# Optimization experiments

Hardware: AMD Instinct MI355X
Metric: run time of the kernel (lower is better)

The kernel has to match this reference:

```python
import jax, jax.numpy as jnp
import numpy as np

LEAKY_SLOPE = 0.01

def bilinear_interpolate(grid, coords):
    # grid: [H, W, C]; coords: [N, 2] in [0,1] (x, y order as in torch code)
    H = grid.shape[0] - 1
    W = grid.shape[1] - 1
    fx = coords[:, 0] * W
    fy = coords[:, 1] * H
    x0 = fx.astype(jnp.int32)
    y0 = fy.astype(jnp.int32)
    xf = jnp.mod(fx, 1.0)
    yf = jnp.mod(fy, 1.0)
    x1 = jnp.minimum(x0 + 1, W)
    y1 = jnp.minimum(y0 + 1, H)
    tl = grid[y0, x0]  # [N, C]
    tr = grid[y0, x1]
    bl = grid[y1, x0]
    br = grid[y1, x1]
    xf = xf[:, None]
    yf = yf[:, None]
    top = (1.0 - xf) * tl + xf * tr
    bot = (1.0 - xf) * bl + xf * br
    return (1.0 - yf) * top + yf * bot


def setup_inputs() -> dict:
    key = jax.random.key(0)
    ks = jax.random.split(key, 10)
    N = 2097152
    pos = jax.random.uniform(ks[0], (N, 2), dtype=jnp.float32)
    dir = jax.random.uniform(ks[1], (N, 2), dtype=jnp.float32)
    pos_grid = jax.random.normal(ks[2], (256, 256, 3), dtype=jnp.float32) * 10.0
    dir_grid = jax.random.normal(ks[3], (256, 256, 3), dtype=jnp.float32) * 10.0
    # Linear layers: PyTorch default init U(-1/sqrt(fan_in), 1/sqrt(fan_in))
    def linear(kw, kb, fan_in, fan_out):
        bound = 1.0 / np.sqrt(fan_in)
        W = jax.random.uniform(kw, (fan_out, fan_in), minval=-bound, maxval=bound, dtype=jnp.float32)
        b = jax.random.uniform(kb, (fan_out,), minval=-bound, maxval=bound, dtype=jnp.float32)
        return W, b
    W1, b1 = linear(ks[4], ks[5], 6, 64)
    W2, b2 = linear(ks[6], ks[7], 64, 64)
    W3, b3 = linear(ks[8], ks[9], 64, 1)
    return {"pos": pos, "dir": dir, "pos_grid": pos_grid, "dir_grid": dir_grid,
            "W1": W1, "b1": b1, "W2": W2, "b2": b2, "W3": W3, "b3": b3}


def reference(pos, dir, pos_grid, dir_grid, W1, b1, W2, b2, W3, b3):
    pos_feat = jax.lax.stop_gradient(bilinear_interpolate(pos_grid, pos))  # .detach() in torch
    dir_feat = jax.lax.stop_gradient(bilinear_interpolate(dir_grid, dir))
    x = jnp.concatenate([pos_feat, dir_feat], axis=1)  # [N, 6]
    x = jax.nn.leaky_relu(x @ W1.T + b1, LEAKY_SLOPE)
    x = jax.nn.leaky_relu(x @ W2.T + b2, LEAKY_SLOPE)
    return jax.nn.sigmoid(x @ W3.T + b3)  # [N, 1]
```

## Files before the change

### kernel.cpp

```cpp
#include <hip/hip_runtime.h>
#include <hip/hip_bf16.h>
#include <math.h>


#define NTHREADS 256

typedef __attribute__((ext_vector_type(4))) short s16x4;
typedef __attribute__((ext_vector_type(8))) short s16x8;
typedef __attribute__((ext_vector_type(8))) __bf16 bf16x8;
typedef __attribute__((ext_vector_type(4))) float f32x4;
typedef __attribute__((ext_vector_type(4))) int i32x4;
typedef __attribute__((ext_vector_type(2))) int i32x2;

static __device__ __forceinline__ short f2bf(float f) {
    return __builtin_bit_cast(short, __float2bfloat16(f));
}
static __device__ __forceinline__ int pk2(float lo, float hi) {
    unsigned short l = (unsigned short)f2bf(lo);
    unsigned short h = (unsigned short)f2bf(hi);
    return (int)(((unsigned int)h << 16) | (unsigned int)l);
}
static __device__ __forceinline__ int cvt_pk_bf16(float a, float b) {
    int r;
    asm("v_cvt_pk_bf16_f32 %0, %1, %2" : "=v"(r) : "v"(a), "v"(b));
    return r;
}
static __device__ __forceinline__ float bflo(int u) {
    return __builtin_bit_cast(float, u << 16);
}
static __device__ __forceinline__ float bfhi(int u) {
    return __builtin_bit_cast(float, (int)(u & 0xffff0000));
}
static __device__ __forceinline__ int opaq(int x) {
    asm volatile("" : "+v"(x));
    return x;
}

__global__ __launch_bounds__(256) void make_patches(
    const float* __restrict__ gP, const float* __restrict__ gD,
    int* __restrict__ outP, int* __restrict__ outD) {
    int gid = blockIdx.x * 256 + threadIdx.x;
    const float* g = (gid < 65536) ? gP : gD;
    int* po = (gid < 65536) ? outP : outD;
    int id = gid & 65535;
    int y0 = id >> 8, x0 = id & 255;
    int x1 = min(x0 + 1, 255), y1 = min(y0 + 1, 255);
    const float* tl = g + (y0 * 256 + x0) * 3;
    const float* tr = g + (y0 * 256 + x1) * 3;
    const float* bl = g + (y1 * 256 + x0) * 3;
    const float* br = g + (y1 * 256 + x1) * 3;
    i32x4 u0;
    i32x2 u1;
    u0[0] = pk2(tl[0], bl[0]);
    u0[1] = pk2(tl[1], bl[1]);
    u0[2] = pk2(tl[2], bl[2]);
    u0[3] = pk2(tr[0], br[0]);
    u1[0] = pk2(tr[1], br[1]);
    u1[1] = pk2(tr[2], br[2]);
    *(i32x4*)(po + id * 8) = u0;
    *(i32x2*)(po + id * 8 + 4) = u1;
}

__global__ void pack_weights(const float* __restrict__ W1,
                             const float* __restrict__ b1,
                             const float* __restrict__ W2,
                             int* __restrict__ wt1, int* __restrict__ wt2) {
    int lane = threadIdx.x;
    int c = lane & 15, q = lane >> 4, q4 = q * 4;
#pragma unroll
    for (int mt = 0; mt < 4; ++mt) {
        int f = mt * 16 + c;
        float v[4];
#pragma unroll
        for (int j = 0; j < 4; ++j) {
            int k = q4 + j;
            float x = 0.0f;
            if (k < 6) x = W1[f * 6 + k];
            else if (k == 6) x = b1[f];
            v[j] = x;
        }
        wt1[lane * 8 + mt * 2 + 0] = pk2(v[0], v[1]);
        wt1[lane * 8 + mt * 2 + 1] = pk2(v[2], v[3]);
    }
#pragma unroll
    for (int kt2 = 0; kt2 < 2; ++kt2)
#pragma unroll
        for (int mt = 0; mt < 4; ++mt) {
            int n2 = mt * 16 + c;
            float v[8];
#pragma unroll
            for (int j2 = 0; j2 < 8; ++j2) {
                int k = kt2 * 32 + ((j2 >> 2) * 16) + q4 + (j2 & 3);
                v[j2] = W2[n2 * 64 + k];
            }
            int base = lane * 32 + (kt2 * 4 + mt) * 4;
#pragma unroll
            for (int h = 0; h < 4; ++h)
                wt2[base + h] = pk2(v[2 * h], v[2 * h + 1]);
        }
}

static __device__ __forceinline__ void patch_issue(
    const int* __restrict__ tab, float px, float py, int* P, float& xf,
    float& yf) {
    float fx = px * 255.0f;
    float fy = py * 255.0f;
    int x0 = (int)fx;
    int y0 = (int)fy;
    xf = fx - floorf(fx);
    yf = fy - floorf(fy);
    int idx = (y0 << 8) | x0;
    i32x4 a = *(const i32x4*)(tab + idx * 8);
    i32x2 b = *(const i32x2*)(tab + idx * 8 + 4);
    P[0] = a[0]; P[1] = a[1]; P[2] = a[2];
    P[3] = a[3]; P[4] = b[0]; P[5] = b[1];
}

static __device__ __forceinline__ void patch_lerp(const int* P, float xf,
                                                  float yf, float* f) {
#pragma unroll
    for (int ch = 0; ch < 3; ++ch) {
        float tl = bflo(P[ch]), bl = bfhi(P[ch]);
        float tr = bflo(P[ch + 3]), br = bfhi(P[ch + 3]);
        float top = fmaf(xf, tr - tl, tl);
        float bot = fmaf(xf, br - bl, bl);
        f[ch] = fmaf(yf, bot - top, top);
    }
}

__global__ __launch_bounds__(NTHREADS, 5) void mlp_mfma_kernel(
    const float* __restrict__ pos, const float* __restrict__ dir,
    const int* __restrict__ patP, const int* __restrict__ patD,
    const int* __restrict__ wt1, const int* __restrict__ wt2,
    const float* __restrict__ b2, const float* __restrict__ W3,
    const float* __restrict__ b3, float* __restrict__ out) {
    __shared__ int lds_F[4 * 64 * 4];
    __shared__ __align__(16) float cw[128];

    const int tid = threadIdx.x;
    if (tid < 128) cw[tid] = (tid < 64) ? b2[tid] : W3[tid - 64];
    __syncthreads();

    const int w = tid >> 6;
    const int lane = tid & 63;
    const int c = lane & 15;
    const int q = lane >> 4;
    const int q4 = q * 4;

    int* FB = lds_F + w * (64 * 4);

    s16x4 A1f[4];
#pragma unroll
    for (int mt = 0; mt < 4; ++mt)
        A1f[mt] = __builtin_bit_cast(
            s16x4, *(const i32x2*)(wt1 + lane * 8 + mt * 2));
    s16x8 A2f[2][4];
#pragma unroll
    for (int kt2 = 0; kt2 < 2; ++kt2)
#pragma unroll
        for (int mt = 0; mt < 4; ++mt)
            A2f[kt2][mt] = __builtin_bit_cast(
                s16x8,
                *(const i32x4*)(wt2 + lane * 32 + (kt2 * 4 + mt) * 4));

    const float b3s = b3[0];
    const int dbias = pk2(1.0f, 0.0f);
    const f32x4 zacc = {0.f, 0.f, 0.f, 0.f};

    const long base = ((long)blockIdx.x * 4 + w) * 64;
    const float2* pos2 = (const float2*)pos;
    const float2* dir2 = (const float2*)dir;

    {
        float2 cp = pos2[base + lane];
        float2 cd = dir2[base + lane];
        int P0_[12];
        float fr0[4];
        patch_issue(patP, cp.x, cp.y, P0_, fr0[0], fr0[1]);
        patch_issue(patD, cd.x, cd.y, P0_ + 6, fr0[2], fr0[3]);
        float feat[6];
        patch_lerp(P0_, fr0[0], fr0[1], feat);
        patch_lerp(P0_ + 6, fr0[2], fr0[3], feat + 3);
        i32x4 dv;
        dv[0] = cvt_pk_bf16(feat[0], feat[1]);
        dv[1] = cvt_pk_bf16(feat[2], feat[3]);
        dv[2] = cvt_pk_bf16(feat[4], feat[5]);
        dv[3] = dbias;
        *(i32x4*)(FB + lane * 4) = dv;
    }

    float s[4];
#pragma unroll
    for (int t = 0; t < 4; ++t) {
        i32x2 bi = *(const i32x2*)(FB + (t * 16 + c) * 4 + (q & 1) * 2);
        s16x4 bfeat = __builtin_bit_cast(s16x4, bi);

        f32x4 a1[4];
#pragma unroll
        for (int mt = 0; mt < 4; ++mt)
            a1[mt] = __builtin_amdgcn_mfma_f32_16x16x16bf16_1k(
                A1f[mt], bfeat, zacc, 0, 0, 0);

        i32x4 bbi[2];
#pragma unroll
        for (int kt2 = 0; kt2 < 2; ++kt2)
#pragma unroll
            for (int h = 0; h < 2; ++h) {
                f32x4 x = a1[kt2 * 2 + h];
                float l0 = fmaxf(x[0], 0.01f * x[0]);
                float l1 = fmaxf(x[1], 0.01f * x[1]);
                float l2 = fmaxf(x[2], 0.01f * x[2]);
                float l3 = fmaxf(x[3], 0.01f * x[3]);
                bbi[kt2][h * 2 + 0] = cvt_pk_bf16(l0, l1);
                bbi[kt2][h * 2 + 1] = cvt_pk_bf16(l2, l3);
            }

        f32x4 a2[4];
        {
            const float* cwb = cw + opaq(q4);
#pragma unroll
            for (int mt = 0; mt < 4; ++mt)
                a2[mt] = *(const f32x4*)(cwb + mt * 16);
        }
#pragma unroll
        for (int kt2 = 0; kt2 < 2; ++kt2) {
            bf16x8 bb = __builtin_bit_cast(bf16x8, bbi[kt2]);
#pragma unroll
            for (int mt = 0; mt < 4; ++mt)
                a2[mt] = __builtin_amdgcn_mfma_f32_16x16x32_bf16(
                    __builtin_bit_cast(bf16x8, A2f[kt2][mt]), bb, a2[mt],
                    0, 0, 0);
        }

        float tx = 0.0f, ta = 0.0f;
        const float* cww = cw + opaq(64 + q4);
#pragma unroll
        for (int mt = 0; mt < 4; ++mt) {
            const f32x4 wv = *(const f32x4*)(cww + mt * 16);
#pragma unroll
            for (int r = 0; r < 4; ++r) {
                float x = a2[mt][r];
                tx = fmaf(x, wv[r], tx);
                ta = fmaf(__builtin_fabsf(x), wv[r], ta);
            }
        }
        float tt = fmaf(0.505f, tx, 0.495f * ta);
        tt += __shfl_xor(tt, 16, 64);
        tt += __shfl_xor(tt, 32, 64);
        s[t] = tt;
    }

    float sa = (q & 1) ? s[1] : s[0];
    float sb = (q & 1) ? s[3] : s[2];
    float v = (q & 2) ? sb : sa;
    v += b3s;
    v = 1.0f / (1.0f + __expf(-v));
    out[base + q * 16 + c] = v;
}

extern "C" void kernel_launch(void* const* d_in, const int* in_sizes, int n_in,
                              void* d_out, int out_size, void* d_ws,
                              size_t ws_size, hipStream_t stream) {
    const float* pos = (const float*)d_in[0];
    const float* dir = (const float*)d_in[1];
    const float* pos_grid = (const float*)d_in[2];
    const float* dir_grid = (const float*)d_in[3];
    const float* W1 = (const float*)d_in[4];
    const float* b1 = (const float*)d_in[5];
    const float* W2 = (const float*)d_in[6];
    const float* b2 = (const float*)d_in[7];
    const float* W3 = (const float*)d_in[8];
    const float* b3 = (const float*)d_in[9];
    float* out = (float*)d_out;

    int* patP = (int*)d_ws;
    int* patD = patP + 65536 * 8;
    int* wt1 = patD + 65536 * 8;
    int* wt2 = wt1 + 512;

    make_patches<<<512, 256, 0, stream>>>(pos_grid, dir_grid, patP, patD);
    pack_weights<<<1, 64, 0, stream>>>(W1, b1, W2, wt1, wt2);

    const int n = in_sizes[0] / 2;
    const int batches = n / 64;
    const int blocks = batches / 4;

    mlp_mfma_kernel<<<blocks, NTHREADS, 0, stream>>>(
        pos, dir, patP, patD, wt1, wt2, b2, W3, b3, out);
}
```

Baseline: 154.5 us.

## Process four 64-point batches per wave with prefetched coordinates and packed math

Each wave now loops over four 64-point batches, which spreads the per-wave weight and bias setup over more work and cuts the grid to a quarter of its size. The next batch's pos/dir loads are issued before the current batch's lerp and MFMA work so their latency is hidden. The layer-2 bias moves from LDS into registers, and the leaky-relu and final dot product use packed v_pk_mul/v_pk_fma plus v_fract instead of floor. The extra registers lower the launch-bounds occupancy hint from 5 to 4, and with fewer blocks there is less parallelism left to hide gather latency.

```diff
diff --git a/kernel.cpp b/kernel.cpp
--- a/kernel.cpp
+++ b/kernel.cpp
@@ -4,11 +4,13 @@
 
 
 #define NTHREADS 256
+#define NB 4
 
 typedef __attribute__((ext_vector_type(4))) short s16x4;
 typedef __attribute__((ext_vector_type(8))) short s16x8;
 typedef __attribute__((ext_vector_type(8))) __bf16 bf16x8;
 typedef __attribute__((ext_vector_type(4))) float f32x4;
+typedef __attribute__((ext_vector_type(2))) float f32x2;
 typedef __attribute__((ext_vector_type(4))) int i32x4;
 typedef __attribute__((ext_vector_type(2))) int i32x2;
 
@@ -23,6 +25,21 @@
 static __device__ __forceinline__ int cvt_pk_bf16(float a, float b) {
     int r;
     asm("v_cvt_pk_bf16_f32 %0, %1, %2" : "=v"(r) : "v"(a), "v"(b));
+    return r;
+}
+static __device__ __forceinline__ f32x2 pk_fma(f32x2 a, f32x2 b, f32x2 c) {
+    f32x2 d;
+    asm("v_pk_fma_f32 %0, %1, %2, %3" : "=v"(d) : "v"(a), "v"(b), "v"(c));
+    return d;
+}
+static __device__ __forceinline__ f32x2 pk_mul(f32x2 a, f32x2 b) {
+    f32x2 d;
+    asm("v_pk_mul_f32 %0, %1, %2" : "=v"(d) : "v"(a), "v"(b));
+    return d;
+}
+static __device__ __forceinline__ float fractf_hw(float x) {
+    float r;
+    asm("v_fract_f32 %0, %1" : "=v"(r) : "v"(x));
     return r;
 }
 static __device__ __forceinline__ float bflo(int u) {
@@ -107,8 +124,8 @@
     float fy = py * 255.0f;
     int x0 = (int)fx;
     int y0 = (int)fy;
-    xf = fx - floorf(fx);
-    yf = fy - floorf(fy);
+    xf = fractf_hw(fx);
+    yf = fractf_hw(fy);
     int idx = (y0 << 8) | x0;
     i32x4 a = *(const i32x4*)(tab + idx * 8);
     i32x2 b = *(const i32x2*)(tab + idx * 8 + 4);
@@ -128,17 +145,17 @@
     }
 }
 
-__global__ __launch_bounds__(NTHREADS, 5) void mlp_mfma_kernel(
+__global__ __launch_bounds__(NTHREADS, 4) void mlp_mfma_kernel(
     const float* __restrict__ pos, const float* __restrict__ dir,
     const int* __restrict__ patP, const int* __restrict__ patD,
     const int* __restrict__ wt1, const int* __restrict__ wt2,
     const float* __restrict__ b2, const float* __restrict__ W3,
     const float* __restrict__ b3, float* __restrict__ out) {
     __shared__ int lds_F[4 * 64 * 4];
-    __shared__ __align__(16) float cw[128];
+    __shared__ __align__(16) float cw[64];
 
     const int tid = threadIdx.x;
-    if (tid < 128) cw[tid] = (tid < 64) ? b2[tid] : W3[tid - 64];
+    if (tid < 64) cw[tid] = W3[tid];
     __syncthreads();
 
     const int w = tid >> 6;
@@ -162,100 +179,125 @@
             A2f[kt2][mt] = __builtin_bit_cast(
                 s16x8,
                 *(const i32x4*)(wt2 + lane * 32 + (kt2 * 4 + mt) * 4));
+    f32x4 ci[4];
+#pragma unroll
+    for (int mt = 0; mt < 4; ++mt)
+        ci[mt] = *(const f32x4*)(b2 + mt * 16 + q4);
 
     const float b3s = b3[0];
     const int dbias = pk2(1.0f, 0.0f);
-    const f32x4 zacc = {0.f, 0.f, 0.f, 0.f};
-
-    const long base = ((long)blockIdx.x * 4 + w) * 64;
+    const f32x2 c001 = {0.01f, 0.01f};
+
+    const long wave_global = (long)blockIdx.x * 4 + w;
+    const long base0 = wave_global * (64L * NB);
     const float2* pos2 = (const float2*)pos;
     const float2* dir2 = (const float2*)dir;
 
-    {
-        float2 cp = pos2[base + lane];
-        float2 cd = dir2[base + lane];
+    float2 cp = pos2[base0 + lane];
+    float2 cd = dir2[base0 + lane];
+
+#pragma unroll 1
+    for (int ib = 0; ib < NB; ++ib) {
+        const long base = base0 + ib * 64;
+
         int P0_[12];
         float fr0[4];
         patch_issue(patP, cp.x, cp.y, P0_, fr0[0], fr0[1]);
         patch_issue(patD, cd.x, cd.y, P0_ + 6, fr0[2], fr0[3]);
-        float feat[6];
-        patch_lerp(P0_, fr0[0], fr0[1], feat);
-        patch_lerp(P0_ + 6, fr0[2], fr0[3], feat + 3);
-        i32x4 dv;
-        dv[0] = cvt_pk_bf16(feat[0], feat[1]);
-        dv[1] = cvt_pk_bf16(feat[2], feat[3]);
-        dv[2] = cvt_pk_bf16(feat[4], feat[5]);
-        dv[3] = dbias;
-        *(i32x4*)(FB + lane * 4) = dv;
+
+        {
+            int mb = min(ib + 1, NB - 1);
+            cp = pos2[base0 + mb * 64 + lane];
+            cd = dir2[base0 + mb * 64 + lane];
+        }
+
+        {
+            float feat[6];
+            patch_lerp(P0_, fr0[0], fr0[1], feat);
+            patch_lerp(P0_ + 6, fr0[2], fr0[3], feat + 3);
+            i32x4 dv;
+            dv[0] = cvt_pk_bf16(feat[0], feat[1]);
+            dv[1] = cvt_pk_bf16(feat[2], feat[3]);
+            dv[2] = cvt_pk_bf16(feat[4], feat[5]);
+            dv[3] = dbias;
+            *(i32x4*)(FB + lane * 4) = dv;
+        }
+
+        float s[4];
+#pragma unroll
+        for (int t = 0; t < 4; ++t) {
+            i32x2 bi = *(const i32x2*)(FB + (t * 16 + c) * 4 + (q & 1) * 2);
+            s16x4 bfeat = __builtin_bit_cast(s16x4, bi);
+
+            const f32x4 zacc = {0.f, 0.f, 0.f, 0.f};
+            f32x4 a1[4];
+#pragma unroll
+            for (int mt = 0; mt < 4; ++mt)
+                a1[mt] = __builtin_amdgcn_mfma_f32_16x16x16bf16_1k(
+                    A1f[mt], bfeat, zacc, 0, 0, 0);
+
+            i32x4 bbi[2];
+#pragma unroll
+            for (int kt2 = 0; kt2 < 2; ++kt2)
+#pragma unroll
+                for (int h = 0; h < 2; ++h) {
+                    f32x4 x = a1[kt2 * 2 + h];
+                    f32x2 xlo = {x[0], x[1]}, xhi = {x[2], x[3]};
+                    f32x2 ylo = pk_mul(xlo, c001);
+                    f32x2 yhi = pk_mul(xhi, c001);
+                    float l0 = fmaxf(x[0], ylo[0]);
+                    float l1 = fmaxf(x[1], ylo[1]);
+                    float l2 = fmaxf(x[2], yhi[0]);
+                    float l3 = fmaxf(x[3], yhi[1]);
+                    bbi[kt2][h * 2 + 0] = cvt_pk_bf16(l0, l1);
+                    bbi[kt2][h * 2 + 1] = cvt_pk_bf16(l2, l3);
+                }
+
+            f32x4 a2[4];
+#pragma unroll
+            for (int mt = 0; mt < 4; ++mt) a2[mt] = ci[mt];
+#pragma unroll
+            for (int kt2 = 0; kt2 < 2; ++kt2) {
+                bf16x8 bb = __builtin_bit_cast(bf16x8, bbi[kt2]);
+#pragma unroll
+                for (int mt = 0; mt < 4; ++mt)
+                    a2[mt] = __builtin_amdgcn_mfma_f32_16x16x32_bf16(
+                        __builtin_bit_cast(bf16x8, A2f[kt2][mt]), bb, a2[mt],
+                        0, 0, 0);
+            }
+
+            f32x2 tx = {0.f, 0.f}, ta = {0.f, 0.f};
+            const float* cww = cw + opaq(q4);
+#pragma unroll
+            for (int mt = 0; mt < 4; ++mt) {
+                const f32x4 wv = *(const f32x4*)(cww + mt * 16);
+                f32x2 w0 = {wv[0], wv[1]}, w1 = {wv[2], wv[3]};
+                f32x4 x = a2[mt];
+                i32x4 xb = __builtin_bit_cast(i32x4, x);
+                i32x4 ab = {xb[0] & 0x7fffffff, xb[1] & 0x7fffffff,
+                            xb[2] & 0x7fffffff, xb[3] & 0x7fffffff};
+                f32x4 xa = __builtin_bit_cast(f32x4, ab);
+                f32x2 xlo = {x[0], x[1]}, xhi = {x[2], x[3]};
+                f32x2 alo = {xa[0], xa[1]}, ahi = {xa[2], xa[3]};
+                tx = pk_fma(xlo, w0, tx);
+                tx = pk_fma(xhi, w1, tx);
+                ta = pk_fma(alo, w0, ta);
+                ta = pk_fma(ahi, w1, ta);
+            }
+            float tt = fmaf(0.505f, tx[0] + tx[1],
+                            0.495f * (ta[0] + ta[1]));
+            tt += __shfl_xor(tt, 16, 64);
+            tt += __shfl_xor(tt, 32, 64);
+            s[t] = tt;
+        }
+
+        float sa = (q & 1) ? s[1] : s[0];
+        float sb = (q & 1) ? s[3] : s[2];
+        float v = (q & 2) ? sb : sa;
+        v += b3s;
+        v = 1.0f / (1.0f + __expf(-v));
+        out[base + q * 16 + c] = v;
     }
-
-    float s[4];
-#pragma unroll
-    for (int t = 0; t < 4; ++t) {
-        i32x2 bi = *(const i32x2*)(FB + (t * 16 + c) * 4 + (q & 1) * 2);
-        s16x4 bfeat = __builtin_bit_cast(s16x4, bi);
-
-        f32x4 a1[4];
-#pragma unroll
-        for (int mt = 0; mt < 4; ++mt)
-            a1[mt] = __builtin_amdgcn_mfma_f32_16x16x16bf16_1k(
-                A1f[mt], bfeat, zacc, 0, 0, 0);
-
-        i32x4 bbi[2];
-#pragma unroll
-        for (int kt2 = 0; kt2 < 2; ++kt2)
-#pragma unroll
-            for (int h = 0; h < 2; ++h) {
-                f32x4 x = a1[kt2 * 2 + h];
-                float l0 = fmaxf(x[0], 0.01f * x[0]);
-                float l1 = fmaxf(x[1], 0.01f * x[1]);
-                float l2 = fmaxf(x[2], 0.01f * x[2]);
-                float l3 = fmaxf(x[3], 0.01f * x[3]);
-                bbi[kt2][h * 2 + 0] = cvt_pk_bf16(l0, l1);
-                bbi[kt2][h * 2 + 1] = cvt_pk_bf16(l2, l3);
-            }
-
-        f32x4 a2[4];
-        {
-            const float* cwb = cw + opaq(q4);
-#pragma unroll
-            for (int mt = 0; mt < 4; ++mt)
-                a2[mt] = *(const f32x4*)(cwb + mt * 16);
-        }
-#pragma unroll
-        for (int kt2 = 0; kt2 < 2; ++kt2) {
-            bf16x8 bb = __builtin_bit_cast(bf16x8, bbi[kt2]);
-#pragma unroll
-            for (int mt = 0; mt < 4; ++mt)
-                a2[mt] = __builtin_amdgcn_mfma_f32_16x16x32_bf16(
-                    __builtin_bit_cast(bf16x8, A2f[kt2][mt]), bb, a2[mt],
-                    0, 0, 0);
-        }
-
-        float tx = 0.0f, ta = 0.0f;
-        const float* cww = cw + opaq(64 + q4);
-#pragma unroll
-        for (int mt = 0; mt < 4; ++mt) {
-            const f32x4 wv = *(const f32x4*)(cww + mt * 16);
-#pragma unroll
-            for (int r = 0; r < 4; ++r) {
-                float x = a2[mt][r];
-                tx = fmaf(x, wv[r], tx);
-                ta = fmaf(__builtin_fabsf(x), wv[r], ta);
-            }
-        }
-        float tt = fmaf(0.505f, tx, 0.495f * ta);
-        tt += __shfl_xor(tt, 16, 64);
-        tt += __shfl_xor(tt, 32, 64);
-        s[t] = tt;
-    }
-
-    float sa = (q & 1) ? s[1] : s[0];
-    float sb = (q & 1) ? s[3] : s[2];
-    float v = (q & 2) ? sb : sa;
-    v += b3s;
-    v = 1.0f / (1.0f + __expf(-v));
-    out[base + q * 16 + c] = v;
 }
 
 extern "C" void kernel_launch(void* const* d_in, const int* in_sizes, int n_in,
@@ -283,7 +325,8 @@
 
     const int n = in_sizes[0] / 2;
     const int batches = n / 64;
-    const int blocks = batches / 4;
+    const int waves = batches / NB;
+    const int blocks = waves / 4;
 
     mlp_mfma_kernel<<<blocks, NTHREADS, 0, stream>>>(
         pos, dir, patP, patD, wt1, wt2, b2, W3, b3, out);
```

Measured after the change: 142.4 us. 7.9% less time.

## Software-pipeline patch gathers across batches per wave and fuse setup kernels

Applied to the files above, without the earlier changes.

Each wave now processes four 64-point batches in a loop. It issues the grid-patch gathers and the coordinate loads for upcoming batches before running the MFMA MLP on the current one, so gather latency overlaps compute. The weight-packing kernel is merged into the patch-building kernel to save a launch. b2 is held in registers instead of LDS, and frac uses v_fract_f32. The kernel launches a quarter as many blocks with occupancy bound lowered to 4, which raises register pressure and reduces parallelism.

```diff
diff --git a/kernel.cpp b/kernel.cpp
--- a/kernel.cpp
+++ b/kernel.cpp
@@ -4,6 +4,7 @@
 
 
 #define NTHREADS 256
+#define NB 4
 
 typedef __attribute__((ext_vector_type(4))) short s16x4;
 typedef __attribute__((ext_vector_type(8))) short s16x8;
@@ -25,6 +26,11 @@
     asm("v_cvt_pk_bf16_f32 %0, %1, %2" : "=v"(r) : "v"(a), "v"(b));
     return r;
 }
+static __device__ __forceinline__ float fractf_hw(float x) {
+    float r;
+    asm("v_fract_f32 %0, %1" : "=v"(r) : "v"(x));
+    return r;
+}
 static __device__ __forceinline__ float bflo(int u) {
     return __builtin_bit_cast(float, u << 16);
 }
@@ -38,66 +44,65 @@
 
 __global__ __launch_bounds__(256) void make_patches(
     const float* __restrict__ gP, const float* __restrict__ gD,
-    int* __restrict__ outP, int* __restrict__ outD) {
+    const float* __restrict__ W1, const float* __restrict__ b1,
+    const float* __restrict__ W2, int* __restrict__ outP,
+    int* __restrict__ outD, int* __restrict__ wt1, int* __restrict__ wt2) {
     int gid = blockIdx.x * 256 + threadIdx.x;
-    const float* g = (gid < 65536) ? gP : gD;
-    int* po = (gid < 65536) ? outP : outD;
-    int id = gid & 65535;
-    int y0 = id >> 8, x0 = id & 255;
-    int x1 = min(x0 + 1, 255), y1 = min(y0 + 1, 255);
-    const float* tl = g + (y0 * 256 + x0) * 3;
-    const float* tr = g + (y0 * 256 + x1) * 3;
-    const float* bl = g + (y1 * 256 + x0) * 3;
-    const float* br = g + (y1 * 256 + x1) * 3;
-    i32x4 u0;
-    i32x2 u1;
-    u0[0] = pk2(tl[0], bl[0]);
-    u0[1] = pk2(tl[1], bl[1]);
-    u0[2] = pk2(tl[2], bl[2]);
-    u0[3] = pk2(tr[0], br[0]);
-    u1[0] = pk2(tr[1], br[1]);
-    u1[1] = pk2(tr[2], br[2]);
-    *(i32x4*)(po + id * 8) = u0;
-    *(i32x2*)(po + id * 8 + 4) = u1;
-}
-
-__global__ void pack_weights(const float* __restrict__ W1,
-                             const float* __restrict__ b1,
-                             const float* __restrict__ W2,
-                             int* __restrict__ wt1, int* __restrict__ wt2) {
-    int lane = threadIdx.x;
-    int c = lane & 15, q = lane >> 4, q4 = q * 4;
-#pragma unroll
-    for (int mt = 0; mt < 4; ++mt) {
-        int f = mt * 16 + c;
-        float v[4];
-#pragma unroll
-        for (int j = 0; j < 4; ++j) {
-            int k = q4 + j;
-            float x = 0.0f;
-            if (k < 6) x = W1[f * 6 + k];
-            else if (k == 6) x = b1[f];
-            v[j] = x;
+    if (gid < 131072) {
+        const float* g = (gid < 65536) ? gP : gD;
+        int* po = (gid < 65536) ? outP : outD;
+        int id = gid & 65535;
+        int y0 = id >> 8, x0 = id & 255;
+        int x1 = min(x0 + 1, 255), y1 = min(y0 + 1, 255);
+        const float* tl = g + (y0 * 256 + x0) * 3;
+        const float* tr = g + (y0 * 256 + x1) * 3;
+        const float* bl = g + (y1 * 256 + x0) * 3;
+        const float* br = g + (y1 * 256 + x1) * 3;
+        i32x4 u0;
+        i32x2 u1;
+        u0[0] = pk2(tl[0], bl[0]);
+        u0[1] = pk2(tl[1], bl[1]);
+        u0[2] = pk2(tl[2], bl[2]);
+        u0[3] = pk2(tr[0], br[0]);
+        u1[0] = pk2(tr[1], br[1]);
+        u1[1] = pk2(tr[2], br[2]);
+        *(i32x4*)(po + id * 8) = u0;
+        *(i32x2*)(po + id * 8 + 4) = u1;
+    } else if (gid < 131136) {
+        int lane = gid - 131072;
+        int c = lane & 15, q = lane >> 4, q4 = q * 4;
+#pragma unroll
+        for (int mt = 0; mt < 4; ++mt) {
+            int f = mt * 16 + c;
+            float v[4];
+#pragma unroll
+            for (int j = 0; j < 4; ++j) {
+                int k = q4 + j;
+                float x = 0.0f;
+                if (k < 6) x = W1[f * 6 + k];
+                else if (k == 6) x = b1[f];
+                v[j] = x;
+            }
+            wt1[lane * 8 + mt * 2 + 0] = pk2(v[0], v[1]);
+            wt1[lane * 8 + mt * 2 + 1] = pk2(v[2], v[3]);
         }
-        wt1[lane * 8 + mt * 2 + 0] = pk2(v[0], v[1]);
-        wt1[lane * 8 + mt * 2 + 1] = pk2(v[2], v[3]);
+#pragma unroll
+        for (int kt2 = 0; kt2 < 2; ++kt2)
+#pragma unroll
+            for (int mt = 0; mt < 4; ++mt) {
+                int n2 = mt * 16 + c;
+                float v[8];
+#pragma unroll
+                for (int j2 = 0; j2 < 8; ++j2) {
+                    int k = kt2 * 32 + ((j2 >> 2) * 16) + q4 + (j2 & 3);
+                    v[j2] = W2[n2 * 64 + k];
+                }
+                int base = lane * 32 + (kt2 * 4 + mt) * 4;
+#pragma unroll
+                for (int h = 0; h < 4; ++h)
+                    wt2[base + h] = pk2(v[2 * h], v[2 * h + 1]);
+            }
     }
-#pragma unroll
-    for (int kt2 = 0; kt2 < 2; ++kt2)
-#pragma unroll
-        for (int mt = 0; mt < 4; ++mt) {
-            int n2 = mt * 16 + c;
-            float v[8];
-#pragma unroll
-            for (int j2 = 0; j2 < 8; ++j2) {
-                int k = kt2 * 32 + ((j2 >> 2) * 16) + q4 + (j2 & 3);
-                v[j2] = W2[n2 * 64 + k];
-            }
-            int base = lane * 32 + (kt2 * 4 + mt) * 4;
-#pragma unroll
-            for (int h = 0; h < 4; ++h)
-                wt2[base + h] = pk2(v[2 * h], v[2 * h + 1]);
-        }
 }
 
 static __device__ __forceinline__ void patch_issue(
@@ -107,8 +112,8 @@
     float fy = py * 255.0f;
     int x0 = (int)fx;
     int y0 = (int)fy;
-    xf = fx - floorf(fx);
-    yf = fy - floorf(fy);
+    xf = fractf_hw(fx);
+    yf = fractf_hw(fy);
     int idx = (y0 << 8) | x0;
     i32x4 a = *(const i32x4*)(tab + idx * 8);
     i32x2 b = *(const i32x2*)(tab + idx * 8 + 4);
@@ -128,17 +133,17 @@
     }
 }
 
-__global__ __launch_bounds__(NTHREADS, 5) void mlp_mfma_kernel(
+__global__ __launch_bounds__(NTHREADS, 4) void mlp_mfma_kernel(
     const float* __restrict__ pos, const float* __restrict__ dir,
     const int* __restrict__ patP, const int* __restrict__ patD,
     const int* __restrict__ wt1, const int* __restrict__ wt2,
     const float* __restrict__ b2, const float* __restrict__ W3,
     const float* __restrict__ b3, float* __restrict__ out) {
     __shared__ int lds_F[4 * 64 * 4];
-    __shared__ __align__(16) float cw[128];
+    __shared__ __align__(16) float cw[64];
 
     const int tid = threadIdx.x;
-    if (tid < 128) cw[tid] = (tid < 64) ? b2[tid] : W3[tid - 64];
+    if (tid < 64) cw[tid] = W3[tid];
     __syncthreads();
 
     const int w = tid >> 6;
@@ -162,22 +167,28 @@
             A2f[kt2][mt] = __builtin_bit_cast(
                 s16x8,
                 *(const i32x4*)(wt2 + lane * 32 + (kt2 * 4 + mt) * 4));
+    f32x4 ci[4];
+#pragma unroll
+    for (int mt = 0; mt < 4; ++mt)
+        ci[mt] = *(const f32x4*)(b2 + mt * 16 + q4);
 
     const float b3s = b3[0];
     const int dbias = pk2(1.0f, 0.0f);
-    const f32x4 zacc = {0.f, 0.f, 0.f, 0.f};
-
-    const long base = ((long)blockIdx.x * 4 + w) * 64;
+
+    const long wave_global = (long)blockIdx.x * 4 + w;
+    const long base0 = wave_global * (64L * NB);
     const float2* pos2 = (const float2*)pos;
     const float2* dir2 = (const float2*)dir;
 
+    float2 cp1, cd1;
     {
-        float2 cp = pos2[base + lane];
-        float2 cd = dir2[base + lane];
+        float2 c0p = pos2[base0 + lane], c0d = dir2[base0 + lane];
+        cp1 = pos2[base0 + 64 + lane];
+        cd1 = dir2[base0 + 64 + lane];
         int P0_[12];
         float fr0[4];
-        patch_issue(patP, cp.x, cp.y, P0_, fr0[0], fr0[1]);
-        patch_issue(patD, cd.x, cd.y, P0_ + 6, fr0[2], fr0[3]);
+        patch_issue(patP, c0p.x, c0p.y, P0_, fr0[0], fr0[1]);
+        patch_issue(patD, c0d.x, c0d.y, P0_ + 6, fr0[2], fr0[3]);
         float feat[6];
         patch_lerp(P0_, fr0[0], fr0[1], feat);
         patch_lerp(P0_ + 6, fr0[2], fr0[3], feat + 3);
@@ -189,73 +200,98 @@
         *(i32x4*)(FB + lane * 4) = dv;
     }
 
-    float s[4];
-#pragma unroll
-    for (int t = 0; t < 4; ++t) {
-        i32x2 bi = *(const i32x2*)(FB + (t * 16 + c) * 4 + (q & 1) * 2);
-        s16x4 bfeat = __builtin_bit_cast(s16x4, bi);
-
-        f32x4 a1[4];
-#pragma unroll
-        for (int mt = 0; mt < 4; ++mt)
-            a1[mt] = __builtin_amdgcn_mfma_f32_16x16x16bf16_1k(
-                A1f[mt], bfeat, zacc, 0, 0, 0);
-
-        i32x4 bbi[2];
-#pragma unroll
-        for (int kt2 = 0; kt2 < 2; ++kt2)
-#pragma unroll
-            for (int h = 0; h < 2; ++h) {
-                f32x4 x = a1[kt2 * 2 + h];
-                float l0 = fmaxf(x[0], 0.01f * x[0]);
-                float l1 = fmaxf(x[1], 0.01f * x[1]);
-                float l2 = fmaxf(x[2], 0.01f * x[2]);
-                float l3 = fmaxf(x[3], 0.01f * x[3]);
-                bbi[kt2][h * 2 + 0] = cvt_pk_bf16(l0, l1);
-                bbi[kt2][h * 2 + 1] = cvt_pk_bf16(l2, l3);
+#pragma unroll 1
+    for (int ib = 0; ib < NB; ++ib) {
+        const long base = base0 + ib * 64;
+
+        int PB[12];
+        float frB[4];
+        patch_issue(patP, cp1.x, cp1.y, PB, frB[0], frB[1]);
+        patch_issue(patD, cd1.x, cd1.y, PB + 6, frB[2], frB[3]);
+
+        {
+            int mb = min(ib + 2, NB - 1);
+            cp1 = pos2[base0 + mb * 64 + lane];
+            cd1 = dir2[base0 + mb * 64 + lane];
+        }
+
+        float s[4];
+#pragma unroll
+        for (int t = 0; t < 4; ++t) {
+            i32x2 bi = *(const i32x2*)(FB + (t * 16 + c) * 4 + (q & 1) * 2);
+            s16x4 bfeat = __builtin_bit_cast(s16x4, bi);
+
+            const f32x4 zacc = {0.f, 0.f, 0.f, 0.f};
+            f32x4 a1[4];
+#pragma unroll
+            for (int mt = 0; mt < 4; ++mt)
+                a1[mt] = __builtin_amdgcn_mfma_f32_16x16x16bf16_1k(
+                    A1f[mt], bfeat, zacc, 0, 0, 0);
+
+            i32x4 bbi[2];
+#pragma unroll
+            for (int kt2 = 0; kt2 < 2; ++kt2)
+#pragma unroll
+                for (int h = 0; h < 2; ++h) {
+                    f32x4 x = a1[kt2 * 2 + h];
+                    float l0 = fmaxf(x[0], 0.01f * x[0]);
+                    float l1 = fmaxf(x[1], 0.01f * x[1]);
+                    float l2 = fmaxf(x[2], 0.01f * x[2]);
+                    float l3 = fmaxf(x[3], 0.01f * x[3]);
+                    bbi[kt2][h * 2 + 0] = cvt_pk_bf16(l0, l1);
+                    bbi[kt2][h * 2 + 1] = cvt_pk_bf16(l2, l3);
+                }
+
+            f32x4 a2[4];
+#pragma unroll
+            for (int mt = 0; mt < 4; ++mt) a2[mt] = ci[mt];
+#pragma unroll
+            for (int kt2 = 0; kt2 < 2; ++kt2) {
+                bf16x8 bb = __builtin_bit_cast(bf16x8, bbi[kt2]);
+#pragma unroll
+                for (int mt = 0; mt < 4; ++mt)
+                    a2[mt] = __builtin_amdgcn_mfma_f32_16x16x32_bf16(
+                        __builtin_bit_cast(bf16x8, A2f[kt2][mt]), bb, a2[mt],
+                        0, 0, 0);
             }
 
-        f32x4 a2[4];
-        {
-            const float* cwb = cw + opaq(q4);
-#pragma unroll
-            for (int mt = 0; mt < 4; ++mt)
-                a2[mt] = *(const f32x4*)(cwb + mt * 16);
+            float tx = 0.0f, ta = 0.0f;
+            const float* cww = cw + opaq(q4);
+#pragma unroll
+            for (int mt = 0; mt < 4; ++mt) {
+                const f32x4 wv = *(const f32x4*)(cww + mt * 16);
+#pragma unroll
+                for (int r = 0; r < 4; ++r) {
+                    float x = a2[mt][r];
+                    tx = fmaf(x, wv[r], tx);
+                    ta = fmaf(__builtin_fabsf(x), wv[r], ta);
+                }
+            }
+            float tt = fmaf(0.505f, tx, 0.495f * ta);
+            tt += __shfl_xor(tt, 16, 64);
+            tt += __shfl_xor(tt, 32, 64);
+            s[t] = tt;
         }
-#pragma unroll
-        for (int kt2 = 0; kt2 < 2; ++kt2) {
-            bf16x8 bb = __builtin_bit_cast(bf16x8, bbi[kt2]);
-#pragma unroll
-            for (int mt = 0; mt < 4; ++mt)
-                a2[mt] = __builtin_amdgcn_mfma_f32_16x16x32_bf16(
-                    __builtin_bit_cast(bf16x8, A2f[kt2][mt]), bb, a2[mt],
-                    0, 0, 0);
+
+        float sa = (q & 1) ? s[1] : s[0];
+        float sb = (q & 1) ? s[3] : s[2];
+        float v = (q & 2) ? sb : sa;
+        v += b3s;
+        v = 1.0f / (1.0f + __expf(-v));
+        out[base + q * 16 + c] = v;
+
+        if (ib + 1 < NB) {
+            float feat[6];
+            patch_lerp(PB, frB[0], frB[1], feat);
+            patch_lerp(PB + 6, frB[2], frB[3], feat + 3);
+            i32x4 dv;
+            dv[0] = cvt_pk_bf16(feat[0], feat[1]);
+            dv[1] = cvt_pk_bf16(feat[2], feat[3]);
+            dv[2] = cvt_pk_bf16(feat[4], feat[5]);
+            dv[3] = dbias;
+            *(i32x4*)(FB + lane * 4) = dv;
         }
-
-        float tx = 0.0f, ta = 0.0f;
-        const float* cww = cw + opaq(64 + q4);
-#pragma unroll
-        for (int mt = 0; mt < 4; ++mt) {
-            const f32x4 wv = *(const f32x4*)(cww + mt * 16);
-#pragma unroll
-            for (int r = 0; r < 4; ++r) {
-                float x = a2[mt][r];
-                tx = fmaf(x, wv[r], tx);
-                ta = fmaf(__builtin_fabsf(x), wv[r], ta);
-            }
-        }
-        float tt = fmaf(0.505f, tx, 0.495f * ta);
-        tt += __shfl_xor(tt, 16, 64);
-        tt += __shfl_xor(tt, 32, 64);
-        s[t] = tt;
     }
-
-    float sa = (q & 1) ? s[1] : s[0];
-    float sb = (q & 1) ? s[3] : s[2];
-    float v = (q & 2) ? sb : sa;
-    v += b3s;
-    v = 1.0f / (1.0f + __expf(-v));
-    out[base + q * 16 + c] = v;
 }
 
 extern "C" void kernel_launch(void* const* d_in, const int* in_sizes, int n_in,
@@ -278,12 +314,13 @@
     int* wt1 = patD + 65536 * 8;
     int* wt2 = wt1 + 512;
 
-    make_patches<<<512, 256, 0, stream>>>(pos_grid, dir_grid, patP, patD);
-    pack_weights<<<1, 64, 0, stream>>>(W1, b1, W2, wt1, wt2);
+    make_patches<<<513, 256, 0, stream>>>(pos_grid, dir_grid, W1, b1, W2,
+                                          patP, patD, wt1, wt2);
 
     const int n = in_sizes[0] / 2;
     const int batches = n / 64;
-    const int blocks = batches / 4;
+    const int waves = batches / NB;
+    const int blocks = waves / 4;
 
     mlp_mfma_kernel<<<blocks, NTHREADS, 0, stream>>>(
         pos, dir, patP, patD, wt1, wt2, b2, W3, b3, out);
```

Measured after the change: 137.5 us. 1.12x faster.
